# Performance work log

Measured on AMD Instinct MI355X. Metric: run time of the kernel, lower is better.

Reference implementation:

```python
import jax, jax.numpy as jnp
import numpy as np

DIM = 768
HEADS = 12
HIDDEN = 3072
EPS = 1e-5  # torch nn.LayerNorm default


def _layer_norm(x, w, b):
    m = jnp.mean(x, axis=-1, keepdims=True)
    v = jnp.mean(jnp.square(x - m), axis=-1, keepdims=True)
    return (x - m) * jax.lax.rsqrt(v + EPS) * w + b


def setup_inputs() -> dict:
    key = jax.random.key(0)
    ks = jax.random.split(key, 10)
    s = lambda fan_in: 1.0 / np.sqrt(fan_in)
    return {
        "x": jax.random.normal(ks[0], (4, 2048, DIM), dtype=jnp.float32),
        "ln1_w": jnp.ones((DIM,), jnp.float32),
        "ln1_b": jnp.zeros((DIM,), jnp.float32),
        "qkv_w": jax.random.normal(ks[1], (3 * DIM, DIM), jnp.float32) * s(DIM),
        "qkv_b": jnp.zeros((3 * DIM,), jnp.float32),
        "proj_w": jax.random.normal(ks[2], (DIM, DIM), jnp.float32) * s(DIM),
        "proj_b": jnp.zeros((DIM,), jnp.float32),
        "ln2_w": jnp.ones((DIM,), jnp.float32),
        "ln2_b": jnp.zeros((DIM,), jnp.float32),
        "fc1_w": jax.random.normal(ks[3], (HIDDEN, DIM), jnp.float32) * s(DIM),
        "fc1_b": jnp.zeros((HIDDEN,), jnp.float32),
        "fc2_w": jax.random.normal(ks[4], (DIM, HIDDEN), jnp.float32) * s(HIDDEN),
        "fc2_b": jnp.zeros((DIM,), jnp.float32),
    }


def _attention(x, qkv_w, qkv_b, proj_w, proj_b):
    B, N, C = x.shape
    H = HEADS
    D = C // H
    scale = D ** -0.5
    qkv = x @ qkv_w.T + qkv_b                       # [B,N,3C]
    qkv = qkv.reshape(B, N, 3, H, D)
    q, k, v = jnp.moveaxis(qkv, 2, 0)               # each [B,N,H,D]
    attn = jnp.einsum("bnhd,bmhd->bhnm", q, k) * scale
    attn = jax.nn.softmax(attn, axis=-1)
    out = jnp.einsum("bhnm,bmhd->bnhd", attn, v).reshape(B, N, C)
    return out @ proj_w.T + proj_b


def reference(x, ln1_w, ln1_b, qkv_w, qkv_b, proj_w, proj_b,
              ln2_w, ln2_b, fc1_w, fc1_b, fc2_w, fc2_b):
    x = x + _attention(_layer_norm(x, ln1_w, ln1_b), qkv_w, qkv_b, proj_w, proj_b)
    h = _layer_norm(x, ln2_w, ln2_b)
    h = jax.nn.gelu(h @ fc1_w.T + fc1_b, approximate=False)
    x = x + (h @ fc2_w.T + fc2_b)
    return x
```

## Files before the change

kernel.cpp:

```cpp
#include <hip/hip_runtime.h>
#include <cstddef>


typedef _Float16 h8 __attribute__((ext_vector_type(8)));
typedef _Float16 h4 __attribute__((ext_vector_type(4)));
typedef _Float16 h2 __attribute__((ext_vector_type(2)));
typedef float f4 __attribute__((ext_vector_type(4)));

#define MFMA16(a, b, c) __builtin_amdgcn_mfma_f32_16x16x32_f16((a), (b), (c), 0, 0, 0)
#define MFMAK16(a, b, c) __builtin_amdgcn_mfma_f32_16x16x16f16((a), (b), (c), 0, 0, 0)

__device__ __forceinline__ _Float16 f2h(float x) { return (_Float16)x; }
__device__ __forceinline__ h2 pk2(float a, float b) {
    return __builtin_bit_cast(h2, __builtin_amdgcn_cvt_pkrtz(a, b));
}
__device__ __forceinline__ h4 pk4(float a, float b, float c, float d) {
    h2 p0 = pk2(a, b);
    h2 p1 = pk2(c, d);
    h4 r; r[0] = p0[0]; r[1] = p0[1]; r[2] = p1[0]; r[3] = p1[1];
    return r;
}

__device__ __forceinline__ void gl_lds16(const _Float16* g, _Float16* l) {
    __builtin_amdgcn_global_load_lds(
        (const __attribute__((address_space(1))) void*)g,
        (__attribute__((address_space(3))) void*)l, 16, 0, 0);
}

__global__ void cvt_all(const float* __restrict__ s0, _Float16* __restrict__ d0, int n0,
                        const float* __restrict__ s1, _Float16* __restrict__ d1, int n1,
                        const float* __restrict__ s2, _Float16* __restrict__ d2, int n2,
                        const float* __restrict__ s3, _Float16* __restrict__ d3) {
    int i = (blockIdx.x * 256 + threadIdx.x) * 4;
    const float* s; _Float16* d; int base;
    if (i < n0) { s = s0; d = d0; base = 0; }
    else if (i < n0 + n1) { s = s1; d = d1; base = n0; }
    else if (i < n0 + n1 + n2) { s = s2; d = d2; base = n0 + n1; }
    else { s = s3; d = d3; base = n0 + n1 + n2; }
    int j = i - base;
    float4 v = *(const float4*)(s + j);
    *(h4*)(d + j) = pk4(v.x, v.y, v.z, v.w);
}

__global__ void ln_f16(const float* __restrict__ x, const float* __restrict__ w,
                       const float* __restrict__ b, _Float16* __restrict__ out) {
    int row = blockIdx.x;
    int tid = threadIdx.x;
    float4 v = ((const float4*)(x + (size_t)row * 768))[tid];
    float s = v.x + v.y + v.z + v.w;
    float s2 = v.x * v.x + v.y * v.y + v.z * v.z + v.w * v.w;
#pragma unroll
    for (int off = 32; off > 0; off >>= 1) {
        s += __shfl_down(s, off, 64);
        s2 += __shfl_down(s2, off, 64);
    }
    __shared__ float red[6];
    if ((tid & 63) == 0) { red[tid >> 6] = s; red[3 + (tid >> 6)] = s2; }
    __syncthreads();
    s = red[0] + red[1] + red[2];
    s2 = red[3] + red[4] + red[5];
    float mean = s * (1.0f / 768.0f);
    float rstd = rsqrtf(s2 * (1.0f / 768.0f) - mean * mean + 1e-5f);
    float4 wv = ((const float4*)w)[tid];
    float4 bv = ((const float4*)b)[tid];
    *(h4*)(out + (size_t)row * 768 + tid * 4) =
        pk4((v.x - mean) * rstd * wv.x + bv.x, (v.y - mean) * rstd * wv.y + bv.y,
            (v.z - mean) * rstd * wv.z + bv.z, (v.w - mean) * rstd * wv.w + bv.w);
}

enum { MODE_QKV = 0, MODE_PROJ = 1, MODE_FC1 = 2, MODE_FC2 = 3 };

template <int MODE, int TM, int TN>
__global__ __launch_bounds__(256, TM == 64 ? 4 : 3) void gemm_bt(
    const _Float16* __restrict__ A, const _Float16* __restrict__ W,
    const float* __restrict__ bias, const float* __restrict__ resid,
    float* __restrict__ outF, _Float16* __restrict__ oq,
    _Float16* __restrict__ okk, _Float16* __restrict__ ov, int K) {
    constexpr int MI = TM / 32;
    constexpr int NI = TN / 32;
    constexpr int AI = TM / 32;
    constexpr int BI = TN / 32;
    __shared__ _Float16 As[TM * 64];
    __shared__ _Float16 Bs[TN * 64];
    int bm = blockIdx.x * TM, bn = blockIdx.y * TN;
    int tid = threadIdx.x;
    int wave = tid >> 6, lane = tid & 63, quad = lane >> 4, l15 = lane & 15;
    int wrow = (wave >> 1) * (TM / 2), wcol = (wave & 1) * (TN / 2);
    int lr = lane >> 3;
    int sw = ((lane & 7) ^ lr) * 8;
    int rsw = (l15 & 7) * 8;
    f4 acc[MI][NI];
#pragma unroll
    for (int mi = 0; mi < MI; mi++)
#pragma unroll
        for (int ni = 0; ni < NI; ni++) acc[mi][ni] = (f4){0.f, 0.f, 0.f, 0.f};

    const _Float16* ApG[AI];
    _Float16* AsL[AI];
#pragma unroll
    for (int i = 0; i < AI; i++) {
        int r = wave * (TM / 4) + i * 8;
        ApG[i] = A + (size_t)(bm + r + lr) * K + sw;
        AsL[i] = As + r * 64;
    }
    const _Float16* WpG[BI];
    _Float16* BsL[BI];
#pragma unroll
    for (int i = 0; i < BI; i++) {
        int r = wave * (TN / 4) + i * 8;
        WpG[i] = W + (size_t)(bn + r + lr) * K + sw;
        BsL[i] = Bs + r * 64;
    }

    for (int k0 = 0; k0 < K; k0 += 64) {
        __syncthreads();
#pragma unroll
        for (int i = 0; i < AI; i++) { gl_lds16(ApG[i], AsL[i]); ApG[i] += 64; }
#pragma unroll
        for (int i = 0; i < BI; i++) { gl_lds16(WpG[i], BsL[i]); WpG[i] += 64; }
        __syncthreads();
#pragma unroll
        for (int ks = 0; ks < 2; ks++) {
            h8 af[MI], bfr[NI];
#pragma unroll
            for (int mi = 0; mi < MI; mi++)
                af[mi] = *(const h8*)&As[(wrow + 16 * mi + l15) * 64 +
                                         (((4 * ks + quad) * 8) ^ rsw)];
#pragma unroll
            for (int ni = 0; ni < NI; ni++)
                bfr[ni] = *(const h8*)&Bs[(wcol + 16 * ni + l15) * 64 +
                                          (((4 * ks + quad) * 8) ^ rsw)];
#pragma unroll
            for (int mi = 0; mi < MI; mi++)
#pragma unroll
                for (int ni = 0; ni < NI; ni++)
                    acc[mi][ni] = MFMA16(af[mi], bfr[ni], acc[mi][ni]);
        }
    }

#pragma unroll
    for (int mi = 0; mi < MI; mi++) {
#pragma unroll
        for (int ni = 0; ni < NI; ni++) {
            int col = bn + wcol + 16 * ni + l15;
            float bc = bias[col];
            int m0 = bm + wrow + 16 * mi + quad * 4;
            float v0 = acc[mi][ni][0] + bc, v1 = acc[mi][ni][1] + bc;
            float v2 = acc[mi][ni][2] + bc, v3 = acc[mi][ni][3] + bc;
            if (MODE == MODE_QKV) {
                int sec = col / 768;
                int rem = col - sec * 768;
                int h = rem >> 6, d = rem & 63;
                int b_ = m0 >> 11, ns = m0 & 2047;
                size_t bh = (size_t)(b_ * 12 + h);
                if (sec == 0) {
                    size_t base = (bh * 2048 + ns) * 64 + d;
                    oq[base] = f2h(v0 * 0.18033688f);
                    oq[base + 64] = f2h(v1 * 0.18033688f);
                    oq[base + 128] = f2h(v2 * 0.18033688f);
                    oq[base + 192] = f2h(v3 * 0.18033688f);
                } else if (sec == 1) {
                    size_t base = (bh * 2048 + ns) * 64 + d;
                    okk[base] = f2h(v0);
                    okk[base + 64] = f2h(v1);
                    okk[base + 128] = f2h(v2);
                    okk[base + 192] = f2h(v3);
                } else {
                    *(h4*)&ov[(bh * 64 + d) * 2048 + ns] = pk4(v0, v1, v2, v3);
                }
            } else if (MODE == MODE_FC1) {
                float g0 = __expf(v0 * (1.5957691f + 0.14295405f * v0 * v0));
                float g1 = __expf(v1 * (1.5957691f + 0.14295405f * v1 * v1));
                float g2 = __expf(v2 * (1.5957691f + 0.14295405f * v2 * v2));
                float g3 = __expf(v3 * (1.5957691f + 0.14295405f * v3 * v3));
                size_t base = (size_t)m0 * 3072 + col;
                oq[base] = f2h(v0 * g0 / (1.f + g0));
                oq[base + 3072] = f2h(v1 * g1 / (1.f + g1));
                oq[base + 6144] = f2h(v2 * g2 / (1.f + g2));
                oq[base + 9216] = f2h(v3 * g3 / (1.f + g3));
            } else {
                size_t idx = (size_t)m0 * 768 + col;
                outF[idx] = v0 + resid[idx];
                outF[idx + 768] = v1 + resid[idx + 768];
                outF[idx + 1536] = v2 + resid[idx + 1536];
                outF[idx + 2304] = v3 + resid[idx + 2304];
            }
        }
    }
}

__global__ __launch_bounds__(256, 3) void attn_kernel(
    const _Float16* __restrict__ Q, const _Float16* __restrict__ Kp,
    const _Float16* __restrict__ Vt, _Float16* __restrict__ O) {
    int bh = blockIdx.x;
    int qt = blockIdx.y;
    int tid = threadIdx.x;
    int wave = tid >> 6, lane = tid & 63, quad = lane >> 4, l15 = lane & 15;
    int lr = lane >> 3;
    int sw = ((lane & 7) ^ lr) * 8;
    int rsw = (l15 & 7) * 8;

    __shared__ _Float16 Ks[2 * 64 * 64];
    __shared__ _Float16 Vs[2 * 64 * 64];

    h8 qf[2][2];
    {
        const _Float16* Qb =
            Q + (((size_t)bh * 2048) + qt * 128 + wave * 32 + l15) * 64 + quad * 8;
#pragma unroll
        for (int qc = 0; qc < 2; qc++)
#pragma unroll
            for (int ks = 0; ks < 2; ks++)
                qf[qc][ks] = *(const h8*)(Qb + qc * 16 * 64 + ks * 32);
    }
    h4 ones4;
#pragma unroll
    for (int j = 0; j < 4; j++) ones4[j] = (_Float16)1.0f;

    f4 Oa[4][2];
    f4 Ls[2];
#pragma unroll
    for (int dc = 0; dc < 4; dc++)
#pragma unroll
        for (int qc = 0; qc < 2; qc++) Oa[dc][qc] = (f4){0.f, 0.f, 0.f, 0.f};
    Ls[0] = (f4){0.f, 0.f, 0.f, 0.f};
    Ls[1] = (f4){0.f, 0.f, 0.f, 0.f};

    const _Float16* Kg = Kp + (size_t)bh * 2048 * 64;
    const _Float16* Vg = Vt + (size_t)bh * 64 * 2048;
    const _Float16* KpG[2];
    const _Float16* VpG[2];
    int rKV[2];
#pragma unroll
    for (int i = 0; i < 2; i++) {
        rKV[i] = wave * 16 + i * 8;
        KpG[i] = Kg + (size_t)(rKV[i] + lr) * 64 + sw;
        VpG[i] = Vg + (size_t)(rKV[i] + lr) * 2048 + sw;
    }

#pragma unroll
    for (int i = 0; i < 2; i++) {
        gl_lds16(KpG[i], Ks + rKV[i] * 64); KpG[i] += 4096;
        gl_lds16(VpG[i], Vs + rKV[i] * 64); VpG[i] += 64;
    }

    for (int it = 0; it < 32; it++) {
        int bufC = (it & 1) * 4096, bufN = ((it & 1) ^ 1) * 4096;
        __syncthreads();
        if (it + 1 < 32) {
#pragma unroll
            for (int i = 0; i < 2; i++) {
                gl_lds16(KpG[i], Ks + bufN + rKV[i] * 64); KpG[i] += 4096;
                gl_lds16(VpG[i], Vs + bufN + rKV[i] * 64); VpG[i] += 64;
            }
        }

        f4 Sa[4][2];
#pragma unroll
        for (int kc = 0; kc < 4; kc++)
#pragma unroll
            for (int qc = 0; qc < 2; qc++) Sa[kc][qc] = (f4){0.f, 0.f, 0.f, 0.f};
#pragma unroll
        for (int ks = 0; ks < 2; ks++) {
            h8 kf[4];
#pragma unroll
            for (int kc = 0; kc < 4; kc++)
                kf[kc] = *(const h8*)&Ks[bufC + (16 * kc + l15) * 64 +
                                         (((4 * ks + quad) * 8) ^ rsw)];
#pragma unroll
            for (int kc = 0; kc < 4; kc++)
#pragma unroll
                for (int qc = 0; qc < 2; qc++)
                    Sa[kc][qc] = MFMA16(kf[kc], qf[qc][ks], Sa[kc][qc]);
        }

        h4 p[4][2];
#pragma unroll
        for (int kc = 0; kc < 4; kc++)
#pragma unroll
            for (int qc = 0; qc < 2; qc++)
                p[kc][qc] = pk4(exp2f(Sa[kc][qc][0]), exp2f(Sa[kc][qc][1]),
                                exp2f(Sa[kc][qc][2]), exp2f(Sa[kc][qc][3]));

#pragma unroll
        for (int kc = 0; kc < 4; kc++) {
            h4 vf4[4];
#pragma unroll
            for (int dc = 0; dc < 4; dc++)
                vf4[dc] = *(const h4*)&Vs[bufC + (16 * dc + l15) * 64 +
                                          (((2 * kc + (quad >> 1)) * 8) ^ rsw) +
                                          (quad & 1) * 4];
#pragma unroll
            for (int dc = 0; dc < 4; dc++)
#pragma unroll
                for (int qc = 0; qc < 2; qc++)
                    Oa[dc][qc] = MFMAK16(vf4[dc], p[kc][qc], Oa[dc][qc]);
#pragma unroll
            for (int qc = 0; qc < 2; qc++)
                Ls[qc] = MFMAK16(ones4, p[kc][qc], Ls[qc]);
        }
    }

    int b_ = bh / 12, h = bh - b_ * 12;
#pragma unroll
    for (int qc = 0; qc < 2; qc++) {
        float inv = 1.0f / Ls[qc][0];
        int n = qt * 128 + wave * 32 + 16 * qc + l15;
        size_t base = ((size_t)b_ * 2048 + n) * 768 + h * 64;
#pragma unroll
        for (int dc = 0; dc < 4; dc++) {
            f4 o = Oa[dc][qc];
            *(h4*)&O[base + 16 * dc + quad * 4] =
                pk4(o[0] * inv, o[1] * inv, o[2] * inv, o[3] * inv);
        }
    }
}

extern "C" void kernel_launch(void* const* d_in, const int* in_sizes, int n_in,
                              void* d_out, int out_size, void* d_ws, size_t ws_size,
                              hipStream_t stream) {
    const float* x      = (const float*)d_in[0];
    const float* ln1_w  = (const float*)d_in[1];
    const float* ln1_b  = (const float*)d_in[2];
    const float* qkv_w  = (const float*)d_in[3];
    const float* qkv_b  = (const float*)d_in[4];
    const float* proj_w = (const float*)d_in[5];
    const float* proj_b = (const float*)d_in[6];
    const float* ln2_w  = (const float*)d_in[7];
    const float* ln2_b  = (const float*)d_in[8];
    const float* fc1_w  = (const float*)d_in[9];
    const float* fc1_b  = (const float*)d_in[10];
    const float* fc2_w  = (const float*)d_in[11];
    const float* fc2_b  = (const float*)d_in[12];
    float* out = (float*)d_out;

    char* ws = (char*)d_ws;
    size_t off = 0;
    _Float16* wqkv  = (_Float16*)(ws + off); off += (size_t)2304 * 768 * 2;
    _Float16* wproj = (_Float16*)(ws + off); off += (size_t)768 * 768 * 2;
    _Float16* wfc1  = (_Float16*)(ws + off); off += (size_t)3072 * 768 * 2;
    _Float16* wfc2  = (_Float16*)(ws + off); off += (size_t)768 * 3072 * 2;
    _Float16* actA  = (_Float16*)(ws + off); off += (size_t)8192 * 768 * 2;
    _Float16* big   = (_Float16*)(ws + off); off += (size_t)8192 * 3072 * 2;
    _Float16* qb = big;
    _Float16* kb = big + (size_t)48 * 2048 * 64;
    _Float16* vb = big + (size_t)2 * 48 * 2048 * 64;
    _Float16* hb = big;

    cvt_all<<<6912, 256, 0, stream>>>(qkv_w, wqkv, 2304 * 768, proj_w, wproj, 768 * 768,
                                      fc1_w, wfc1, 3072 * 768, fc2_w, wfc2);

    ln_f16<<<8192, 192, 0, stream>>>(x, ln1_w, ln1_b, actA);
    gemm_bt<MODE_QKV, 128, 192><<<dim3(64, 12), 256, 0, stream>>>(actA, wqkv, qkv_b, nullptr,
                                                                  nullptr, qb, kb, vb, 768);
    attn_kernel<<<dim3(48, 16), 256, 0, stream>>>(qb, kb, vb, actA);
    gemm_bt<MODE_PROJ, 64, 128><<<dim3(128, 6), 256, 0, stream>>>(actA, wproj, proj_b, x, out,
                                                                  nullptr, nullptr, nullptr, 768);
    ln_f16<<<8192, 192, 0, stream>>>(out, ln2_w, ln2_b, actA);
    gemm_bt<MODE_FC1, 128, 128><<<dim3(64, 24), 256, 0, stream>>>(actA, wfc1, fc1_b, nullptr,
                                                                  nullptr, hb, nullptr, nullptr, 768);
    gemm_bt<MODE_FC2, 64, 128><<<dim3(128, 6), 256, 0, stream>>>(hb, wfc2, fc2_b, out, out,
                                                                 nullptr, nullptr, nullptr, 3072);
}
```

Before: 356.0 us.

## Split attention over KV halves with combine kernel; widen FC GEMM tiles

Attention is split along the key/value sequence into two halves via a third grid dimension. Each half writes unnormalized partial outputs, scaled by 1/64, plus row sums, and a new combine kernel adds them and normalizes. Launch bounds are raised to allow more resident blocks. This doubles the block count so the 768-block grid fills the GPU better, at the cost of an extra pass over partial outputs in memory. Separately, the FC1 and FC2 GEMMs switch to 192-wide N tiles with fewer grid columns.

```diff
diff --git a/kernel.cpp b/kernel.cpp
--- a/kernel.cpp
+++ b/kernel.cpp
@@ -189,11 +189,13 @@
     }
 }
 
-__global__ __launch_bounds__(256, 3) void attn_kernel(
+__global__ __launch_bounds__(256, 5) void attn_kernel(
     const _Float16* __restrict__ Q, const _Float16* __restrict__ Kp,
-    const _Float16* __restrict__ Vt, _Float16* __restrict__ O) {
+    const _Float16* __restrict__ Vt, _Float16* __restrict__ O0p,
+    _Float16* __restrict__ O1p, float* __restrict__ Lp) {
     int bh = blockIdx.x;
     int qt = blockIdx.y;
+    int sp = blockIdx.z;
     int tid = threadIdx.x;
     int wave = tid >> 6, lane = tid & 63, quad = lane >> 4, l15 = lane & 15;
     int lr = lane >> 3;
@@ -226,8 +228,8 @@
     Ls[0] = (f4){0.f, 0.f, 0.f, 0.f};
     Ls[1] = (f4){0.f, 0.f, 0.f, 0.f};
 
-    const _Float16* Kg = Kp + (size_t)bh * 2048 * 64;
-    const _Float16* Vg = Vt + (size_t)bh * 64 * 2048;
+    const _Float16* Kg = Kp + (size_t)bh * 2048 * 64 + (size_t)sp * 1024 * 64;
+    const _Float16* Vg = Vt + (size_t)bh * 64 * 2048 + sp * 1024;
     const _Float16* KpG[2];
     const _Float16* VpG[2];
     int rKV[2];
@@ -244,10 +246,10 @@
         gl_lds16(VpG[i], Vs + rKV[i] * 64); VpG[i] += 64;
     }
 
-    for (int it = 0; it < 32; it++) {
+    for (int it = 0; it < 16; it++) {
         int bufC = (it & 1) * 4096, bufN = ((it & 1) ^ 1) * 4096;
         __syncthreads();
-        if (it + 1 < 32) {
+        if (it + 1 < 16) {
 #pragma unroll
             for (int i = 0; i < 2; i++) {
                 gl_lds16(KpG[i], Ks + bufN + rKV[i] * 64); KpG[i] += 4096;
@@ -301,19 +303,37 @@
         }
     }
 
-    int b_ = bh / 12, h = bh - b_ * 12;
+    _Float16* Op = (sp == 0 ? O0p : O1p);
 #pragma unroll
     for (int qc = 0; qc < 2; qc++) {
-        float inv = 1.0f / Ls[qc][0];
         int n = qt * 128 + wave * 32 + 16 * qc + l15;
-        size_t base = ((size_t)b_ * 2048 + n) * 768 + h * 64;
+        size_t rbase = ((size_t)bh * 2048 + n) * 64;
 #pragma unroll
         for (int dc = 0; dc < 4; dc++) {
             f4 o = Oa[dc][qc];
-            *(h4*)&O[base + 16 * dc + quad * 4] =
-                pk4(o[0] * inv, o[1] * inv, o[2] * inv, o[3] * inv);
-        }
-    }
+            *(h4*)&Op[rbase + 16 * dc + quad * 4] =
+                pk4(o[0] * 0.015625f, o[1] * 0.015625f, o[2] * 0.015625f, o[3] * 0.015625f);
+        }
+        if (quad == 0) Lp[(size_t)sp * 98304 + (size_t)bh * 2048 + n] = Ls[qc][0];
+    }
+}
+
+__global__ void attn_combine(const _Float16* __restrict__ O0p,
+                             const _Float16* __restrict__ O1p,
+                             const float* __restrict__ Lp,
+                             _Float16* __restrict__ O) {
+    int gid = blockIdx.x * 256 + threadIdx.x;
+    int idx = gid >> 4;
+    int dg = (gid & 15) * 4;
+    int bh = idx >> 11, n = idx & 2047;
+    size_t pbase = (size_t)idx * 64 + dg;
+    h4 a = *(const h4*)&O0p[pbase];
+    h4 b = *(const h4*)&O1p[pbase];
+    float inv = 64.0f / (Lp[idx] + Lp[98304 + idx]);
+    int b_ = bh / 12, h = bh - b_ * 12;
+    *(h4*)&O[((size_t)b_ * 2048 + n) * 768 + h * 64 + dg] =
+        pk4(((float)a[0] + (float)b[0]) * inv, ((float)a[1] + (float)b[1]) * inv,
+            ((float)a[2] + (float)b[2]) * inv, ((float)a[3] + (float)b[3]) * inv);
 }
 
 extern "C" void kernel_launch(void* const* d_in, const int* in_sizes, int n_in,
@@ -342,9 +362,12 @@
     _Float16* wfc2  = (_Float16*)(ws + off); off += (size_t)768 * 3072 * 2;
     _Float16* actA  = (_Float16*)(ws + off); off += (size_t)8192 * 768 * 2;
     _Float16* big   = (_Float16*)(ws + off); off += (size_t)8192 * 3072 * 2;
+    _Float16* O0p   = (_Float16*)(ws + off); off += (size_t)48 * 2048 * 64 * 2;
+    float*    Lp    = (float*)(ws + off);    off += (size_t)2 * 48 * 2048 * 4;
     _Float16* qb = big;
     _Float16* kb = big + (size_t)48 * 2048 * 64;
     _Float16* vb = big + (size_t)2 * 48 * 2048 * 64;
+    _Float16* O1p = big + (size_t)3 * 48 * 2048 * 64;
     _Float16* hb = big;
 
     cvt_all<<<6912, 256, 0, stream>>>(qkv_w, wqkv, 2304 * 768, proj_w, wproj, 768 * 768,
@@ -353,12 +376,13 @@
     ln_f16<<<8192, 192, 0, stream>>>(x, ln1_w, ln1_b, actA);
     gemm_bt<MODE_QKV, 128, 192><<<dim3(64, 12), 256, 0, stream>>>(actA, wqkv, qkv_b, nullptr,
                                                                   nullptr, qb, kb, vb, 768);
-    attn_kernel<<<dim3(48, 16), 256, 0, stream>>>(qb, kb, vb, actA);
+    attn_kernel<<<dim3(48, 16, 2), 256, 0, stream>>>(qb, kb, vb, O0p, O1p, Lp);
+    attn_combine<<<6144, 256, 0, stream>>>(O0p, O1p, Lp, actA);
     gemm_bt<MODE_PROJ, 64, 128><<<dim3(128, 6), 256, 0, stream>>>(actA, wproj, proj_b, x, out,
                                                                   nullptr, nullptr, nullptr, 768);
     ln_f16<<<8192, 192, 0, stream>>>(out, ln2_w, ln2_b, actA);
-    gemm_bt<MODE_FC1, 128, 128><<<dim3(64, 24), 256, 0, stream>>>(actA, wfc1, fc1_b, nullptr,
+    gemm_bt<MODE_FC1, 128, 192><<<dim3(64, 16), 256, 0, stream>>>(actA, wfc1, fc1_b, nullptr,
                                                                   nullptr, hb, nullptr, nullptr, 768);
-    gemm_bt<MODE_FC2, 64, 128><<<dim3(128, 6), 256, 0, stream>>>(hb, wfc2, fc2_b, out, out,
+    gemm_bt<MODE_FC2, 64, 192><<<dim3(128, 4), 256, 0, stream>>>(hb, wfc2, fc2_b, out, out,
                                                                  nullptr, nullptr, nullptr, 3072);
 }
```

New measurement: 521.1 us. 46.4% more time.
